# Optimization experiments

Hardware: AMD Instinct MI355X
Metric: run time of the kernel (lower is better)

The kernel has to match this reference:

```python
import jax, jax.numpy as jnp
import numpy as np


def setup_inputs() -> dict:
    key = jax.random.key(0)
    k1, k2, k3, k4, k5 = jax.random.split(key, 5)
    TOKENS, D_IN, D_OUT = 8192, 4096, 16384
    x = jax.random.normal(k1, (TOKENS, D_IN), dtype=jnp.float32)
    # int8-valued quantized weight/bias stored as int32 (same math)
    q_weight = jax.random.randint(k2, (D_OUT, D_IN), -127, 128, dtype=jnp.int32)
    q_bias = jax.random.randint(k3, (D_OUT,), -127, 128, dtype=jnp.int32)
    scale = jax.random.uniform(k4, (1,), dtype=jnp.float32) * 0.02 + 1e-3
    bias_scale = jax.random.uniform(k5, (1,), dtype=jnp.float32) * 0.02 + 1e-3
    return {"x": x, "q_weight": q_weight, "q_bias": q_bias,
            "scale": scale, "bias_scale": bias_scale}


def reference(x, q_weight, q_bias, scale, bias_scale):
    # Dequantize: weight = q_weight.float() * scale  -> [D_OUT, D_IN]
    weight = q_weight.astype(jnp.float32) * scale[0]
    bias = q_bias.astype(jnp.float32) * bias_scale[0]
    # F.linear(x, weight, bias) = x @ weight.T + bias
    return jnp.einsum('td,od->to', x, weight) + bias
```

## Files before the change

### kernel.cpp

```cpp
#include <hip/hip_runtime.h>
#include <hip/hip_bf16.h>
#include <cstdint>
#include <cstddef>


typedef __bf16 v8bf  __attribute__((ext_vector_type(8)));
typedef float  f32x4 __attribute__((ext_vector_type(4)));

constexpr int M = 8192;
constexpr int N = 16384;
constexpr int K = 4096;
constexpr int BM = 128, BN = 128, BK = 32;

__device__ __forceinline__ unsigned f2bf(float f) {
  union { float f; unsigned u; } v; v.f = f;
  return (v.u + 0x7fffu + ((v.u >> 16) & 1u)) >> 16;
}


__global__ __launch_bounds__(256) void cvt_x_bf16(const float4* __restrict__ in,
                                                  uint2* __restrict__ out) {
  size_t i = (size_t)blockIdx.x * 256 + threadIdx.x;
  float4 a = in[i];
  uint2 o;
  o.x = f2bf(a.x) | (f2bf(a.y) << 16);
  o.y = f2bf(a.z) | (f2bf(a.w) << 16);
  out[i] = o;
}

__global__ __launch_bounds__(256) void cvt_w_bf16(const int4* __restrict__ in,
                                                  uint2* __restrict__ out) {
  size_t i = (size_t)blockIdx.x * 256 + threadIdx.x;
  int4 a = in[i];
  uint2 o;
  o.x = f2bf((float)a.x) | (f2bf((float)a.y) << 16);
  o.y = f2bf((float)a.z) | (f2bf((float)a.w) << 16);
  out[i] = o;
}


__global__ __launch_bounds__(256) void gemm_bt(const __bf16* __restrict__ A,
                                               const __bf16* __restrict__ B,
                                               const int* __restrict__ qbias,
                                               const float* __restrict__ scale,
                                               const float* __restrict__ bscale,
                                               float* __restrict__ C) {
  __shared__ __bf16 As[BM * BK];
  __shared__ __bf16 Bs[BN * BK];

  const int t    = threadIdx.x;
  const int wave = t >> 6;
  const int lane = t & 63;
  const int quad = lane >> 4;
  const int l16  = lane & 15;
  const int m0   = blockIdx.y * BM;
  const int n0   = blockIdx.x * BN;
  const int wm   = (wave & 1) * 64;
  const int wn   = (wave >> 1) * 64;

  const int srow = t >> 2;
  const int scol = (t & 3) * 8;
  const __bf16* gA = A + (size_t)(m0 + srow) * K + scol;
  const __bf16* gB = B + (size_t)(n0 + srow) * K + scol;
  __bf16* lA = As + wave * 512;
  __bf16* lB = Bs + wave * 512;

  f32x4 acc[4][4] = {};

  for (int k0 = 0; k0 < K; k0 += BK) {
    __syncthreads();
    __builtin_amdgcn_global_load_lds((const __attribute__((address_space(1))) void*)gA,
                                     (__attribute__((address_space(3))) void*)lA, 16, 0, 0);
    __builtin_amdgcn_global_load_lds((const __attribute__((address_space(1))) void*)(gA + (size_t)64 * K),
                                     (__attribute__((address_space(3))) void*)(lA + 2048), 16, 0, 0);
    __builtin_amdgcn_global_load_lds((const __attribute__((address_space(1))) void*)gB,
                                     (__attribute__((address_space(3))) void*)lB, 16, 0, 0);
    __builtin_amdgcn_global_load_lds((const __attribute__((address_space(1))) void*)(gB + (size_t)64 * K),
                                     (__attribute__((address_space(3))) void*)(lB + 2048), 16, 0, 0);
    gA += BK; gB += BK;
    __syncthreads();

    v8bf a[4], b[4];
#pragma unroll
    for (int i = 0; i < 4; ++i) {
      a[i] = *(const v8bf*)(As + (wm + i * 16 + l16) * BK + quad * 8);
      b[i] = *(const v8bf*)(Bs + (wn + i * 16 + l16) * BK + quad * 8);
    }
#pragma unroll
    for (int im = 0; im < 4; ++im)
#pragma unroll
      for (int in = 0; in < 4; ++in)
        acc[im][in] = __builtin_amdgcn_mfma_f32_16x16x32_bf16(a[im], b[in], acc[im][in], 0, 0, 0);
  }

  const float s  = scale[0];
  const float bs = bscale[0];
#pragma unroll
  for (int in = 0; in < 4; ++in) {
    const int col = n0 + wn + in * 16 + l16;
    const float bias = (float)qbias[col] * bs;
#pragma unroll
    for (int im = 0; im < 4; ++im) {
      const int row = m0 + wm + im * 16 + quad * 4;
      float* cp = C + (size_t)row * N + col;
#pragma unroll
      for (int r = 0; r < 4; ++r)
        cp[(size_t)r * N] = acc[im][in][r] * s + bias;
    }
  }
}


__device__ __forceinline__ uint4 packf(float4 x, float4 y) {
  uint4 o;
  o.x = f2bf(x.x) | (f2bf(x.y) << 16);
  o.y = f2bf(x.z) | (f2bf(x.w) << 16);
  o.z = f2bf(y.x) | (f2bf(y.y) << 16);
  o.w = f2bf(y.z) | (f2bf(y.w) << 16);
  return o;
}
__device__ __forceinline__ uint4 packi(int4 x, int4 y) {
  uint4 o;
  o.x = f2bf((float)x.x) | (f2bf((float)x.y) << 16);
  o.y = f2bf((float)x.z) | (f2bf((float)x.w) << 16);
  o.z = f2bf((float)y.x) | (f2bf((float)y.y) << 16);
  o.w = f2bf((float)y.z) | (f2bf((float)y.w) << 16);
  return o;
}

__global__ __launch_bounds__(256) void gemm_fused(const float* __restrict__ A32,
                                                  const int* __restrict__ W32,
                                                  const int* __restrict__ qbias,
                                                  const float* __restrict__ scale,
                                                  const float* __restrict__ bscale,
                                                  float* __restrict__ C) {
  __shared__ __bf16 As[BM * BK];
  __shared__ __bf16 Bs[BN * BK];

  const int t    = threadIdx.x;
  const int wave = t >> 6;
  const int lane = t & 63;
  const int quad = lane >> 4;
  const int l16  = lane & 15;
  const int m0   = blockIdx.y * BM;
  const int n0   = blockIdx.x * BN;
  const int wm   = (wave & 1) * 64;
  const int wn   = (wave >> 1) * 64;

  const int srow = t >> 1;
  const int sh   = (t & 1) * 16;
  const float* gA = A32 + (size_t)(m0 + srow) * K + sh;
  const int*   gW = W32 + (size_t)(n0 + srow) * K + sh;
  __bf16* wA = As + srow * BK + sh;
  __bf16* wB = Bs + srow * BK + sh;

  f32x4 acc[4][4] = {};

  for (int k0 = 0; k0 < K; k0 += BK) {
    float4 a0 = *(const float4*)(gA + 0);
    float4 a1 = *(const float4*)(gA + 4);
    float4 a2 = *(const float4*)(gA + 8);
    float4 a3 = *(const float4*)(gA + 12);
    int4 b0 = *(const int4*)(gW + 0);
    int4 b1 = *(const int4*)(gW + 4);
    int4 b2 = *(const int4*)(gW + 8);
    int4 b3 = *(const int4*)(gW + 12);
    gA += BK; gW += BK;
    __syncthreads();
    ((uint4*)wA)[0] = packf(a0, a1);
    ((uint4*)wA)[1] = packf(a2, a3);
    ((uint4*)wB)[0] = packi(b0, b1);
    ((uint4*)wB)[1] = packi(b2, b3);
    __syncthreads();

    v8bf a[4], b[4];
#pragma unroll
    for (int i = 0; i < 4; ++i) {
      a[i] = *(const v8bf*)(As + (wm + i * 16 + l16) * BK + quad * 8);
      b[i] = *(const v8bf*)(Bs + (wn + i * 16 + l16) * BK + quad * 8);
    }
#pragma unroll
    for (int im = 0; im < 4; ++im)
#pragma unroll
      for (int in = 0; in < 4; ++in)
        acc[im][in] = __builtin_amdgcn_mfma_f32_16x16x32_bf16(a[im], b[in], acc[im][in], 0, 0, 0);
  }

  const float s  = scale[0];
  const float bs = bscale[0];
#pragma unroll
  for (int in = 0; in < 4; ++in) {
    const int col = n0 + wn + in * 16 + l16;
    const float bias = (float)qbias[col] * bs;
#pragma unroll
    for (int im = 0; im < 4; ++im) {
      const int row = m0 + wm + im * 16 + quad * 4;
      float* cp = C + (size_t)row * N + col;
#pragma unroll
      for (int r = 0; r < 4; ++r)
        cp[(size_t)r * N] = acc[im][in][r] * s + bias;
    }
  }
}

extern "C" void kernel_launch(void* const* d_in, const int* in_sizes, int n_in,
                              void* d_out, int out_size, void* d_ws, size_t ws_size,
                              hipStream_t stream) {
  const float* x      = (const float*)d_in[0];
  const int*   qw     = (const int*)d_in[1];
  const int*   qbias  = (const int*)d_in[2];
  const float* scale  = (const float*)d_in[3];
  const float* bscale = (const float*)d_in[4];
  float* out = (float*)d_out;

  const size_t needA = (size_t)M * K * sizeof(__bf16);
  const size_t needB = (size_t)N * K * sizeof(__bf16);
  dim3 grid(N / BN, M / BM);

  if (ws_size >= needA + needB) {
    __bf16* wsA = (__bf16*)d_ws;
    __bf16* wsB = wsA + (size_t)M * K;
    cvt_x_bf16<<<(int)((size_t)M * K / (4 * 256)), 256, 0, stream>>>(
        (const float4*)x, (uint2*)wsA);
    cvt_w_bf16<<<(int)((size_t)N * K / (4 * 256)), 256, 0, stream>>>(
        (const int4*)qw, (uint2*)wsB);
    gemm_bt<<<grid, 256, 0, stream>>>(wsA, wsB, qbias, scale, bscale, out);
  } else {
    gemm_fused<<<grid, 256, 0, stream>>>(x, qw, qbias, scale, bscale, out);
  }
}
```

Before: 1.958 ms.

## Replace bf16 GEMM with 256x256 double-buffered, swizzled 8-wave pipelined kernel

Replaces the 128x128 single-buffered GEMM with a 256x256-tile, 512-thread kernel. It double-buffers 64-wide K tiles in LDS and interleaves async global-to-LDS loads with MFMA phases, using barriers, s_setprio and explicit vmcnt waits. It also XOR-swizzles the LDS layout to avoid bank conflicts and remaps block IDs for better L2 locality. The intent is to hide memory latency and raise data reuse per tile. The cost is more LDS use (128KB per block) and more accumulator registers, which may limit occupancy.

```diff
diff --git a/kernel.cpp b/kernel.cpp
--- a/kernel.cpp
+++ b/kernel.cpp
@@ -10,7 +10,7 @@
 constexpr int M = 8192;
 constexpr int N = 16384;
 constexpr int K = 4096;
-constexpr int BM = 128, BN = 128, BK = 32;
+constexpr int NT = K / 64;
 
 __device__ __forceinline__ unsigned f2bf(float f) {
   union { float f; unsigned u; } v; v.f = f;
@@ -39,77 +39,150 @@
 }
 
 
-__global__ __launch_bounds__(256) void gemm_bt(const __bf16* __restrict__ A,
-                                               const __bf16* __restrict__ B,
-                                               const int* __restrict__ qbias,
-                                               const float* __restrict__ scale,
-                                               const float* __restrict__ bscale,
-                                               float* __restrict__ C) {
-  __shared__ __bf16 As[BM * BK];
-  __shared__ __bf16 Bs[BN * BK];
+#define GLD16(G, L) __builtin_amdgcn_global_load_lds(                        \
+    (const __attribute__((address_space(1))) void*)(G),                      \
+    (__attribute__((address_space(3))) void*)(L), 16, 0, 0)
+
+template<int CUR, int KH, int MH, bool DOB>
+__device__ __forceinline__ void phase_loads(const __bf16* As, const __bf16* Bs,
+                                            int aBase, int bBase,
+                                            v8bf (&a)[4], v8bf (&b)[4]) {
+  if constexpr (DOB) {
+#pragma unroll
+    for (int j = 0; j < 4; ++j)
+      b[j] = *(const v8bf*)(Bs + CUR * 16384 + KH * 8192 + bBase + j * 512);
+  }
+#pragma unroll
+  for (int i = 0; i < 4; ++i)
+    a[i] = *(const v8bf*)(As + CUR * 16384 + KH * 8192 + MH * 2048 + aBase + i * 512);
+}
+
+template<int MH>
+__device__ __forceinline__ void phase_mfma(v8bf (&a)[4], v8bf (&b)[4],
+                                           f32x4 (&acc)[8][4]) {
+  __builtin_amdgcn_s_setprio(1);
+#pragma unroll
+  for (int i = 0; i < 4; ++i)
+#pragma unroll
+    for (int j = 0; j < 4; ++j)
+      acc[MH * 4 + i][j] =
+          __builtin_amdgcn_mfma_f32_16x16x32_bf16(a[i], b[j], acc[MH * 4 + i][j], 0, 0, 0);
+  __builtin_amdgcn_s_setprio(0);
+}
+
+#define STAGE_A(BUF, KH, KOFF) do {                                          \
+    GLD16(pA0 + (KOFF), As + (BUF) * 16384 + (KH) * 8192 + wave * 512);      \
+    GLD16(pA1 + (KOFF), As + (BUF) * 16384 + (KH) * 8192 + 4096 + wave * 512); \
+  } while (0)
+#define STAGE_B(BUF, KH, KOFF) do {                                          \
+    GLD16(pB0 + (KOFF), Bs + (BUF) * 16384 + (KH) * 8192 + wave * 512);      \
+    GLD16(pB1 + (KOFF), Bs + (BUF) * 16384 + (KH) * 8192 + 4096 + wave * 512); \
+  } while (0)
+
+#define BAR() __builtin_amdgcn_s_barrier()
+
+#define TILE_BODY(CUR, NXT, KA, KB) do {                                     \
+    phase_loads<CUR, 0, 0, true>(As, Bs, aBase, bBase, a, b);                \
+    STAGE_A(NXT, 1, (KA) + 32);                                              \
+    BAR();                                                                   \
+    phase_mfma<0>(a, b, acc);                                                \
+    BAR();                                                                   \
+    phase_loads<CUR, 0, 1, false>(As, Bs, aBase, bBase, a, b);               \
+    STAGE_B(NXT, 1, (KA) + 32);                                              \
+    BAR();                                                                   \
+    phase_mfma<1>(a, b, acc);                                                \
+    BAR();                                                                   \
+    phase_loads<CUR, 1, 0, true>(As, Bs, aBase, bBase, a, b);                \
+    STAGE_A(CUR, 0, (KB));                                                   \
+    BAR();                                                                   \
+    phase_mfma<0>(a, b, acc);                                                \
+    BAR();                                                                   \
+    phase_loads<CUR, 1, 1, false>(As, Bs, aBase, bBase, a, b);               \
+    STAGE_B(CUR, 0, (KB));                                                   \
+    BAR();                                                                   \
+    phase_mfma<1>(a, b, acc);                                                \
+    asm volatile("s_waitcnt vmcnt(4)" ::: "memory");                         \
+    BAR();                                                                   \
+  } while (0)
+
+__global__ __launch_bounds__(512, 2) void gemm_bt8(const __bf16* __restrict__ A,
+                                                   const __bf16* __restrict__ B,
+                                                   const int* __restrict__ qbias,
+                                                   const float* __restrict__ scale,
+                                                   const float* __restrict__ bscale,
+                                                   float* __restrict__ C) {
+  __shared__ __bf16 As[2 * 2 * 8192];
+  __shared__ __bf16 Bs[2 * 2 * 8192];
 
   const int t    = threadIdx.x;
   const int wave = t >> 6;
   const int lane = t & 63;
   const int quad = lane >> 4;
   const int l16  = lane & 15;
-  const int m0   = blockIdx.y * BM;
-  const int n0   = blockIdx.x * BN;
-  const int wm   = (wave & 1) * 64;
-  const int wn   = (wave >> 1) * 64;
-
-  const int srow = t >> 2;
-  const int scol = (t & 3) * 8;
-  const __bf16* gA = A + (size_t)(m0 + srow) * K + scol;
-  const __bf16* gB = B + (size_t)(n0 + srow) * K + scol;
-  __bf16* lA = As + wave * 512;
-  __bf16* lB = Bs + wave * 512;
-
-  f32x4 acc[4][4] = {};
-
-  for (int k0 = 0; k0 < K; k0 += BK) {
-    __syncthreads();
-    __builtin_amdgcn_global_load_lds((const __attribute__((address_space(1))) void*)gA,
-                                     (__attribute__((address_space(3))) void*)lA, 16, 0, 0);
-    __builtin_amdgcn_global_load_lds((const __attribute__((address_space(1))) void*)(gA + (size_t)64 * K),
-                                     (__attribute__((address_space(3))) void*)(lA + 2048), 16, 0, 0);
-    __builtin_amdgcn_global_load_lds((const __attribute__((address_space(1))) void*)gB,
-                                     (__attribute__((address_space(3))) void*)lB, 16, 0, 0);
-    __builtin_amdgcn_global_load_lds((const __attribute__((address_space(1))) void*)(gB + (size_t)64 * K),
-                                     (__attribute__((address_space(3))) void*)(lB + 2048), 16, 0, 0);
-    gA += BK; gB += BK;
-    __syncthreads();
-
-    v8bf a[4], b[4];
-#pragma unroll
-    for (int i = 0; i < 4; ++i) {
-      a[i] = *(const v8bf*)(As + (wm + i * 16 + l16) * BK + quad * 8);
-      b[i] = *(const v8bf*)(Bs + (wn + i * 16 + l16) * BK + quad * 8);
-    }
-#pragma unroll
-    for (int im = 0; im < 4; ++im)
-#pragma unroll
-      for (int in = 0; in < 4; ++in)
-        acc[im][in] = __builtin_amdgcn_mfma_f32_16x16x32_bf16(a[im], b[in], acc[im][in], 0, 0, 0);
-  }
+  const int wr   = wave >> 2;
+  const int wc   = wave & 3;
+
+  const int bid = blockIdx.x;
+  const int wgs = ((bid & 7) << 8) | (bid >> 3);
+  const int bx  = wgs & 63;
+  const int by  = wgs >> 6;
+  const int m0  = by * 256;
+  const int n0  = bx * 256;
+
+  const int pseg  = (((l16 & 1) << 2) | quad) ^ (l16 >> 1);
+  const int aBase = (wr * 64 + (l16 >> 1)) * 64 + pseg * 8;
+  const int bBase = (wc * 32 + (l16 >> 1)) * 64 + pseg * 8;
+
+  const int pr0 = t >> 3;
+  const int ls0 = (t & 7) ^ (pr0 & 7);
+  const int r0  = pr0 * 2 + (ls0 >> 2);
+  const int c80 = ls0 & 3;
+  const __bf16* pA0 = A + (size_t)(m0 + r0) * K + c80 * 8;
+  const __bf16* pA1 = pA0 + (size_t)128 * K;
+  const __bf16* pB0 = B + (size_t)(n0 + r0) * K + c80 * 8;
+  const __bf16* pB1 = pB0 + (size_t)128 * K;
+
+  f32x4 acc[8][4] = {};
+  v8bf a[4], b[4];
+
+  STAGE_A(0, 0, 0);
+  STAGE_B(0, 0, 0);
+  STAGE_A(0, 1, 32);
+  STAGE_B(0, 1, 32);
+  STAGE_A(1, 0, 64);
+  STAGE_B(1, 0, 64);
+  asm volatile("s_waitcnt vmcnt(4)" ::: "memory");
+  BAR();
+
+  for (int tt = 0; tt < NT; tt += 2) {
+    const int ka  = (tt + 1) * 64;
+    const int kb  = (tt + 2 < NT) ? (tt + 2) * 64 : 0;
+    TILE_BODY(0, 1, ka, kb);
+    const int ka2 = kb;
+    const int kb2 = (tt + 3 < NT) ? (tt + 3) * 64 : 0;
+    TILE_BODY(1, 0, ka2, kb2);
+  }
+  asm volatile("s_waitcnt vmcnt(0)" ::: "memory");
 
   const float s  = scale[0];
   const float bs = bscale[0];
 #pragma unroll
-  for (int in = 0; in < 4; ++in) {
-    const int col = n0 + wn + in * 16 + l16;
+  for (int j = 0; j < 4; ++j) {
+    const int col = n0 + wc * 64 + j * 16 + l16;
     const float bias = (float)qbias[col] * bs;
 #pragma unroll
-    for (int im = 0; im < 4; ++im) {
-      const int row = m0 + wm + im * 16 + quad * 4;
+    for (int im = 0; im < 8; ++im) {
+      const int row = m0 + wr * 128 + im * 16 + quad * 4;
       float* cp = C + (size_t)row * N + col;
 #pragma unroll
       for (int r = 0; r < 4; ++r)
-        cp[(size_t)r * N] = acc[im][in][r] * s + bias;
+        cp[(size_t)r * N] = acc[im][j][r] * s + bias;
     }
   }
 }
 
+
+constexpr int FBM = 128, FBN = 128, FBK = 32;
 
 __device__ __forceinline__ uint4 packf(float4 x, float4 y) {
   uint4 o;
@@ -134,16 +207,16 @@
                                                   const float* __restrict__ scale,
                                                   const float* __restrict__ bscale,
                                                   float* __restrict__ C) {
-  __shared__ __bf16 As[BM * BK];
-  __shared__ __bf16 Bs[BN * BK];
+  __shared__ __bf16 As[FBM * FBK];
+  __shared__ __bf16 Bs[FBN * FBK];
 
   const int t    = threadIdx.x;
   const int wave = t >> 6;
   const int lane = t & 63;
   const int quad = lane >> 4;
   const int l16  = lane & 15;
-  const int m0   = blockIdx.y * BM;
-  const int n0   = blockIdx.x * BN;
+  const int m0   = blockIdx.y * FBM;
+  const int n0   = blockIdx.x * FBN;
   const int wm   = (wave & 1) * 64;
   const int wn   = (wave >> 1) * 64;
 
@@ -151,12 +224,12 @@
   const int sh   = (t & 1) * 16;
   const float* gA = A32 + (size_t)(m0 + srow) * K + sh;
   const int*   gW = W32 + (size_t)(n0 + srow) * K + sh;
-  __bf16* wA = As + srow * BK + sh;
-  __bf16* wB = Bs + srow * BK + sh;
+  __bf16* wA = As + srow * FBK + sh;
+  __bf16* wB = Bs + srow * FBK + sh;
 
   f32x4 acc[4][4] = {};
 
-  for (int k0 = 0; k0 < K; k0 += BK) {
+  for (int k0 = 0; k0 < K; k0 += FBK) {
     float4 a0 = *(const float4*)(gA + 0);
     float4 a1 = *(const float4*)(gA + 4);
     float4 a2 = *(const float4*)(gA + 8);
@@ -165,7 +238,7 @@
     int4 b1 = *(const int4*)(gW + 4);
     int4 b2 = *(const int4*)(gW + 8);
     int4 b3 = *(const int4*)(gW + 12);
-    gA += BK; gW += BK;
+    gA += FBK; gW += FBK;
     __syncthreads();
     ((uint4*)wA)[0] = packf(a0, a1);
     ((uint4*)wA)[1] = packf(a2, a3);
@@ -176,8 +249,8 @@
     v8bf a[4], b[4];
 #pragma unroll
     for (int i = 0; i < 4; ++i) {
-      a[i] = *(const v8bf*)(As + (wm + i * 16 + l16) * BK + quad * 8);
-      b[i] = *(const v8bf*)(Bs + (wn + i * 16 + l16) * BK + quad * 8);
+      a[i] = *(const v8bf*)(As + (wm + i * 16 + l16) * FBK + quad * 8);
+      b[i] = *(const v8bf*)(Bs + (wn + i * 16 + l16) * FBK + quad * 8);
     }
 #pragma unroll
     for (int im = 0; im < 4; ++im)
@@ -215,7 +288,6 @@
 
   const size_t needA = (size_t)M * K * sizeof(__bf16);
   const size_t needB = (size_t)N * K * sizeof(__bf16);
-  dim3 grid(N / BN, M / BM);
 
   if (ws_size >= needA + needB) {
     __bf16* wsA = (__bf16*)d_ws;
@@ -224,8 +296,10 @@
         (const float4*)x, (uint2*)wsA);
     cvt_w_bf16<<<(int)((size_t)N * K / (4 * 256)), 256, 0, stream>>>(
         (const int4*)qw, (uint2*)wsB);
-    gemm_bt<<<grid, 256, 0, stream>>>(wsA, wsB, qbias, scale, bscale, out);
+    gemm_bt8<<<dim3((M / 256) * (N / 256)), dim3(512), 0, stream>>>(
+        wsA, wsB, qbias, scale, bscale, out);
   } else {
+    dim3 grid(N / FBN, M / FBM);
     gemm_fused<<<grid, 256, 0, stream>>>(x, qw, qbias, scale, bscale, out);
   }
 }
```

After: 1.921 ms. No clear change (-1.9%).
